# Performance work log

Hardware: AMD Instinct MI355X
Metric: run time of the kernel (lower is better)

## Reference

```python
import jax, jax.numpy as jnp
import numpy as np

N = 100000   # n_nodes (= ninput, identity features)
E = 1600000  # edges per adjacency (avg degree 16)
H = 128      # nhid
EPS = 1e-12


def setup_inputs() -> dict:
    key = jax.random.key(0)
    ks = jax.random.split(key, 24)
    inp = {
        'adj1_rows': jax.random.randint(ks[0], (E,), 0, N),
        'adj1_cols': jax.random.randint(ks[1], (E,), 0, N),
        'adj1_vals': jax.random.uniform(ks[2], (E,), jnp.float32) / 16.0,
        'adj2_rows': jax.random.randint(ks[3], (E,), 0, N),
        'adj2_cols': jax.random.randint(ks[4], (E,), 0, N),
        'adj2_vals': jax.random.uniform(ks[5], (E,), jnp.float32) / 16.0,
    }
    s = 1.0 / np.sqrt(H)
    inp['w1'] = jax.random.uniform(ks[6], (N, H), jnp.float32, -s, s)
    for i in range(2, 10):
        inp[f'w{i}'] = jax.random.uniform(ks[5 + i], (H, H), jnp.float32, -s, s)
    s2 = 1.0 / np.sqrt(2 * H)
    inp['m1'] = jax.random.uniform(ks[15], (H, 2 * H), jnp.float32, -s, s)
    inp['b1'] = jnp.zeros((2 * H,), jnp.float32)
    inp['m2'] = jax.random.uniform(ks[16], (2 * H, 2 * H), jnp.float32, -s2, s2)
    inp['b2'] = jnp.zeros((2 * H,), jnp.float32)
    inp['m3'] = jax.random.uniform(ks[17], (2 * H, 1), jnp.float32, -s2, s2)
    inp['b3'] = jnp.zeros((1,), jnp.float32)
    return inp


def _spmm(rows, cols, vals, x):
    # sparse [N,N] @ dense [N,H] via gather + segment_sum
    return jax.ops.segment_sum(vals[:, None] * x[cols], rows, num_segments=N)


def _l2norm(x):
    # F.normalize(x, p=2, dim=1)
    n = jnp.sqrt(jnp.sum(x * x, axis=1, keepdims=True))
    return x / jnp.maximum(n, EPS)


def _mlp(x, m1, b1, m2, b2, m3, b3):
    # dropout inactive (eval mode) for deterministic reference
    h = jax.nn.relu(x @ m1 + b1)
    h = jax.nn.relu(h @ m2 + b2)
    return h @ m3 + b3  # [N,1]


def _branch(rows, cols, vals, w1, ws, mlp_params):
    x = jax.nn.relu(_spmm(rows, cols, vals, w1))
    x = _l2norm(x)
    score = _mlp(x, *mlp_params)
    for i, w in enumerate(ws):
        x = jax.nn.relu(_spmm(rows, cols, vals, x @ w))
        if i < len(ws) - 1:  # last layer (gc9) is relu only, no normalize
            x = _l2norm(x)
        score = score + _mlp(x, *mlp_params)
    return score


def reference(adj1_rows, adj1_cols, adj1_vals, adj2_rows, adj2_cols, adj2_vals,
              w1, w2, w3, w4, w5, w6, w7, w8, w9,
              m1, b1, m2, b2, m3, b3):
    ws = [w2, w3, w4, w5, w6, w7, w8, w9]
    mlp_params = (m1, b1, m2, b2, m3, b3)
    score1 = _branch(adj1_rows, adj1_cols, adj1_vals, w1, ws, mlp_params)
    score2 = _branch(adj2_rows, adj2_cols, adj2_vals, w1, ws, mlp_params)
    return score1 * score2  # [N,1]
```

## Files before the change

kernel.cpp:

```cpp
#include <hip/hip_runtime.h>
#include <hip/hip_fp16.h>

#define NN 100000
#define NE 1600000
#define HD 128
#define HD2 256

typedef unsigned int u32;
typedef unsigned short u16;
typedef _Float16 half8 __attribute__((ext_vector_type(8)));
typedef float floatx4 __attribute__((ext_vector_type(4)));

static inline int cdiv(int a, int b){ return (a + b - 1) / b; }

__device__ __forceinline__ u32 split_pack(float v){
  __half h;
  if(fabsf(v) < 6.103515625e-05f) h = __ushort_as_half((u16)0);
  else h = __float2half_rn(v);
  float hf = __half2float(h);
  __half l = __float2half_rn((v - hf) * 4096.0f);
  return (u32)__half_as_ushort(h) | ((u32)__half_as_ushort(l) << 16);
}

__global__ void k_zero_int(int* __restrict__ p, int n){
  int i = blockIdx.x * 256 + threadIdx.x;
  if(i < n) p[i] = 0;
}

__global__ void k_zero_f(float* __restrict__ p, int n){
  int i = blockIdx.x * 256 + threadIdx.x;
  if(i < n) p[i] = 0.f;
}

__global__ void k_hist2(const int* __restrict__ r0, const int* __restrict__ r1,
                        int* __restrict__ cnt){
  int e = blockIdx.x * 256 + threadIdx.x;
  if(e < NE){
    const int* rows = blockIdx.y ? r1 : r0;
    atomicAdd(&cnt[blockIdx.y * NN + rows[e]], 1);
  }
}

__global__ void k_scan1b(const int* __restrict__ cnt, int* __restrict__ p0,
                         int* __restrict__ p1, int* __restrict__ sums, int n){
  __shared__ int sh[256];
  int z = blockIdx.y;
  const int* c = cnt + z * n;
  int* part = z ? p1 : p0;
  int* sm = sums + z * 128;
  int tid = threadIdx.x;
  int base = blockIdx.x * 1024 + tid * 4;
  int v0 = (base + 0 < n) ? c[base + 0] : 0;
  int v1 = (base + 1 < n) ? c[base + 1] : 0;
  int v2 = (base + 2 < n) ? c[base + 2] : 0;
  int v3 = (base + 3 < n) ? c[base + 3] : 0;
  int s = v0 + v1 + v2 + v3;
  sh[tid] = s;
  __syncthreads();
  for(int d = 1; d < 256; d <<= 1){
    int t = (tid >= d) ? sh[tid - d] : 0;
    __syncthreads();
    sh[tid] += t;
    __syncthreads();
  }
  int excl = sh[tid] - s;
  if(tid == 255) sm[blockIdx.x] = sh[255];
  if(base + 0 < n) part[base + 0] = excl;
  if(base + 1 < n) part[base + 1] = excl + v0;
  if(base + 2 < n) part[base + 2] = excl + v0 + v1;
  if(base + 3 < n) part[base + 3] = excl + v0 + v1 + v2;
}

__global__ void k_scan2b(int* __restrict__ sums, int nb){
  __shared__ int sh[128];
  int* s = sums + blockIdx.x * 128;
  int tid = threadIdx.x;
  int v = (tid < nb) ? s[tid] : 0;
  sh[tid] = v;
  __syncthreads();
  for(int d = 1; d < 128; d <<= 1){
    int t = (tid >= d) ? sh[tid - d] : 0;
    __syncthreads();
    sh[tid] += t;
    __syncthreads();
  }
  if(tid < nb) s[tid] = sh[tid] - v;
}

__global__ void k_scan3b(int* __restrict__ r0, int* __restrict__ r1,
                         int* __restrict__ cursor, const int* __restrict__ sums, int n){
  int z = blockIdx.y;
  int* rowptr = z ? r1 : r0;
  int* cur = cursor + z * n;
  int off = sums[z * 128 + blockIdx.x];
  int tid = threadIdx.x;
  int base = blockIdx.x * 1024 + tid * 4;
  #pragma unroll
  for(int j = 0; j < 4; j++){
    int idx = base + j;
    if(idx < n){ int r = rowptr[idx] + off; rowptr[idx] = r; cur[idx] = r; }
  }
  if(blockIdx.x == 0 && tid == 0) rowptr[n] = NE;
}

__global__ void k_scatter2(const int* __restrict__ r0, const int* __restrict__ c0,
                           const float* __restrict__ v0,
                           const int* __restrict__ r1, const int* __restrict__ c1,
                           const float* __restrict__ v1,
                           int* __restrict__ cursor,
                           int* __restrict__ oc0, float* __restrict__ ov0,
                           int* __restrict__ oc1, float* __restrict__ ov1){
  int e = blockIdx.x * 256 + threadIdx.x;
  if(e < NE){
    int z = blockIdx.y;
    const int* rows = z ? r1 : r0;
    const int* cols = z ? c1 : c0;
    const float* vals = z ? v1 : v0;
    int* cur = cursor + z * NN;
    int* ocol = z ? oc1 : oc0;
    float* oval = z ? ov1 : ov0;
    int r = rows[e];
    int pp = atomicAdd(&cur[r], 1);
    ocol[pp] = cols[e];
    oval[pp] = vals[e];
  }
}

__global__ void k_splitw(const float* __restrict__ W, u32* __restrict__ out,
                         int K, int N, int total){
  int idx = blockIdx.x * 256 + threadIdx.x;
  if(idx < total){
    int n = idx / K, k = idx - n * K;
    out[idx] = split_pack(W[(size_t)k * N + n]);
  }
}

template<bool NORM>
__global__ void k_spmm(const int* __restrict__ rp0, const int* __restrict__ col0,
                       const float* __restrict__ val0,
                       const int* __restrict__ rp1, const int* __restrict__ col1,
                       const float* __restrict__ val1,
                       const float* __restrict__ X0, const float* __restrict__ X1,
                       u32* __restrict__ outpk){
  int z = blockIdx.z;
  const int* rowptr = z ? rp1 : rp0;
  const int* col    = z ? col1 : col0;
  const float* val  = z ? val1 : val0;
  const float* X    = z ? X1 : X0;
  int node = (blockIdx.x << 2) + (threadIdx.x >> 6);
  int lane = threadIdx.x & 63;
  if(node >= NN) return;
  int s = rowptr[node], e = rowptr[node + 1];
  float ax = 0.f, ay = 0.f, bx = 0.f, by = 0.f;
  float cx = 0.f, cy = 0.f, dx = 0.f, dy = 0.f;
  int i = s;
  for(; i + 15 < e; i += 16){
    int c[16]; float v[16]; float2 xx[16];
    #pragma unroll
    for(int j = 0; j < 16; j++){ c[j] = col[i + j]; v[j] = val[i + j]; }
    #pragma unroll
    for(int j = 0; j < 16; j++) xx[j] = *(const float2*)(X + (size_t)c[j] * HD + lane * 2);
    #pragma unroll
    for(int j = 0; j < 16; j += 4){
      ax += v[j] * xx[j].x + v[j+1] * xx[j+1].x;
      ay += v[j] * xx[j].y + v[j+1] * xx[j+1].y;
      bx += v[j+2] * xx[j+2].x + v[j+3] * xx[j+3].x;
      by += v[j+2] * xx[j+2].y + v[j+3] * xx[j+3].y;
    }
  }
  for(; i + 3 < e; i += 4){
    int   e0 = col[i],   e1 = col[i + 1], e2 = col[i + 2], e3 = col[i + 3];
    float f0 = val[i],   f1 = val[i + 1], f2 = val[i + 2], f3 = val[i + 3];
    float2 x0 = *(const float2*)(X + (size_t)e0 * HD + lane * 2);
    float2 x1 = *(const float2*)(X + (size_t)e1 * HD + lane * 2);
    float2 x2 = *(const float2*)(X + (size_t)e2 * HD + lane * 2);
    float2 x3 = *(const float2*)(X + (size_t)e3 * HD + lane * 2);
    ax += f0 * x0.x + f1 * x1.x;  ay += f0 * x0.y + f1 * x1.y;
    bx += f2 * x2.x + f3 * x3.x;  by += f2 * x2.y + f3 * x3.y;
  }
  for(; i < e; i++){
    int c = col[i]; float v = val[i];
    float2 xv = *(const float2*)(X + (size_t)c * HD + lane * 2);
    ax += v * xv.x; ay += v * xv.y;
  }
  ax += bx + cx + dx;
  ay += by + cy + dy;
  ax = fmaxf(ax, 0.f);
  ay = fmaxf(ay, 0.f);
  if(NORM){
    float ss = ax * ax + ay * ay;
    #pragma unroll
    for(int o = 32; o >= 1; o >>= 1) ss += __shfl_xor(ss, o, 64);
    float scale = 1.f / fmaxf(sqrtf(ss), 1e-12f);
    ax *= scale; ay *= scale;
  }
  size_t gnode = (size_t)(z * NN + node);
  *(uint2*)(outpk + gnode * HD + lane * 2) = make_uint2(split_pack(ax), split_pack(ay));
}

template<int MODE>
__launch_bounds__(256, 2)
__global__ void k_mfma_gemm(const u32* __restrict__ Apk, const u32* __restrict__ Btpk,
                            const float* __restrict__ bias, float* __restrict__ Yout,
                            u32* __restrict__ Hout, const float* __restrict__ m3,
                            float* __restrict__ score, int M, int K, int N){
  __shared__ unsigned short As_h[128 * 40], As_l[128 * 40];
  __shared__ unsigned short Bs_h[128 * 40], Bs_l[128 * 40];
  const int tid = threadIdx.x;
  const int lane = tid & 63, wid = tid >> 6;
  const int lm = lane & 15, lg = lane >> 4;
  const int mq = (wid & 1) * 64, nq = (wid >> 1) * 64;
  const int m0 = blockIdx.x * 128, n0 = blockIdx.y * 128;

  floatx4 accA[4][4], accB[4][4];
  #pragma unroll
  for(int i = 0; i < 4; i++)
    #pragma unroll
    for(int j = 0; j < 4; j++){
      accA[i][j] = (floatx4){0.f, 0.f, 0.f, 0.f};
      accB[i][j] = (floatx4){0.f, 0.f, 0.f, 0.f};
    }

  for(int k0 = 0; k0 < K; k0 += 32){
    uint4 av[4], bv[4];
    #pragma unroll
    for(int j = 0; j < 4; j++){
      int li = tid + j * 256;
      int row = li >> 3, kc = (li & 7) * 4;
      int ar = m0 + row; if(ar >= M) ar = M - 1;
      av[j] = *(const uint4*)(Apk + (size_t)ar * K + k0 + kc);
      bv[j] = *(const uint4*)(Btpk + (size_t)(n0 + row) * K + k0 + kc);
    }
    __syncthreads();
    #pragma unroll
    for(int j = 0; j < 4; j++){
      int li = tid + j * 256;
      int row = li >> 3, kc = (li & 7) * 4;
      int base = row * 40 + kc;
      ushort4 h, l;
      h.x = (u16)(av[j].x & 0xffff); l.x = (u16)(av[j].x >> 16);
      h.y = (u16)(av[j].y & 0xffff); l.y = (u16)(av[j].y >> 16);
      h.z = (u16)(av[j].z & 0xffff); l.z = (u16)(av[j].z >> 16);
      h.w = (u16)(av[j].w & 0xffff); l.w = (u16)(av[j].w >> 16);
      *(ushort4*)&As_h[base] = h;
      *(ushort4*)&As_l[base] = l;
      h.x = (u16)(bv[j].x & 0xffff); l.x = (u16)(bv[j].x >> 16);
      h.y = (u16)(bv[j].y & 0xffff); l.y = (u16)(bv[j].y >> 16);
      h.z = (u16)(bv[j].z & 0xffff); l.z = (u16)(bv[j].z >> 16);
      h.w = (u16)(bv[j].w & 0xffff); l.w = (u16)(bv[j].w >> 16);
      *(ushort4*)&Bs_h[base] = h;
      *(ushort4*)&Bs_l[base] = l;
    }
    __syncthreads();

    half8 fa_h[4], fa_l[4], fb_h[4], fb_l[4];
    #pragma unroll
    for(int s = 0; s < 4; s++){
      int ra = (mq + s * 16 + lm) * 40 + lg * 8;
      fa_h[s] = *(const half8*)&As_h[ra];
      fa_l[s] = *(const half8*)&As_l[ra];
      int rb = (nq + s * 16 + lm) * 40 + lg * 8;
      fb_h[s] = *(const half8*)&Bs_h[rb];
      fb_l[s] = *(const half8*)&Bs_l[rb];
    }
    #pragma unroll
    for(int i = 0; i < 4; i++)
      #pragma unroll
      for(int j = 0; j < 4; j++){
        accA[i][j] = __builtin_amdgcn_mfma_f32_16x16x32_f16(fa_h[i], fb_h[j], accA[i][j], 0, 0, 0);
        accB[i][j] = __builtin_amdgcn_mfma_f32_16x16x32_f16(fa_h[i], fb_l[j], accB[i][j], 0, 0, 0);
        accB[i][j] = __builtin_amdgcn_mfma_f32_16x16x32_f16(fa_l[i], fb_h[j], accB[i][j], 0, 0, 0);
      }
  }

  const float inv4096 = 1.f / 4096.f;
  if(MODE == 0){
    #pragma unroll
    for(int i = 0; i < 4; i++)
      #pragma unroll
      for(int r = 0; r < 4; r++){
        int m = m0 + mq + i * 16 + lg * 4 + r;
        if(m < M){
          #pragma unroll
          for(int j = 0; j < 4; j++){
            int c = n0 + nq + j * 16 + lm;
            Yout[(size_t)m * N + c] = accA[i][j][r] + accB[i][j][r] * inv4096;
          }
        }
      }
  } else if(MODE == 1){
    #pragma unroll
    for(int i = 0; i < 4; i++)
      #pragma unroll
      for(int r = 0; r < 4; r++){
        int m = m0 + mq + i * 16 + lg * 4 + r;
        if(m < M){
          #pragma unroll
          for(int j = 0; j < 4; j++){
            int c = n0 + nq + j * 16 + lm;
            float v = fmaxf(accA[i][j][r] + accB[i][j][r] * inv4096 + bias[c], 0.f);
            Hout[(size_t)m * N + c] = split_pack(v);
          }
        }
      }
  } else {
    #pragma unroll
    for(int i = 0; i < 4; i++)
      #pragma unroll
      for(int r = 0; r < 4; r++){
        float s = 0.f;
        #pragma unroll
        for(int j = 0; j < 4; j++){
          int c = n0 + nq + j * 16 + lm;
          float v = fmaxf(accA[i][j][r] + accB[i][j][r] * inv4096 + bias[c], 0.f);
          s = fmaf(v, m3[c], s);
        }
        s += __shfl_xor(s, 1, 64);
        s += __shfl_xor(s, 2, 64);
        s += __shfl_xor(s, 4, 64);
        s += __shfl_xor(s, 8, 64);
        int m = m0 + mq + i * 16 + lg * 4 + r;
        if(lm == 0 && m < M) atomicAdd(&score[m], s);
      }
  }
}

__global__ void k_final(const float* __restrict__ sc, const float* __restrict__ b3,
                        float* __restrict__ out){
  int i = blockIdx.x * 256 + threadIdx.x;
  if(i < NN){
    float b = 9.f * b3[0];
    out[i] = (sc[i] + b) * (sc[NN + i] + b);
  }
}

extern "C" void kernel_launch(void* const* d_in, const int* in_sizes, int n_in,
                              void* d_out, int out_size, void* d_ws, size_t ws_size,
                              hipStream_t stream){
  const int*   a1r = (const int*)d_in[0];
  const int*   a1c = (const int*)d_in[1];
  const float* a1v = (const float*)d_in[2];
  const int*   a2r = (const int*)d_in[3];
  const int*   a2c = (const int*)d_in[4];
  const float* a2v = (const float*)d_in[5];
  const float* w1  = (const float*)d_in[6];
  const float* w[8];
  for(int i = 0; i < 8; i++) w[i] = (const float*)d_in[7 + i];
  const float* m1 = (const float*)d_in[15];
  const float* b1 = (const float*)d_in[16];
  const float* m2 = (const float*)d_in[17];
  const float* b2 = (const float*)d_in[18];
  const float* m3 = (const float*)d_in[19];
  const float* b3 = (const float*)d_in[20];
  float* out = (float*)d_out;

  char* base = (char*)d_ws;
  size_t off = 0;
  auto alloc = [&](size_t bytes) -> char* {
    char* r = base + off;
    off += (bytes + 255) & ~(size_t)255;
    return r;
  };
  int*   c1ptr = (int*)  alloc((size_t)(NN + 1) * 4);
  int*   c1col = (int*)  alloc((size_t)NE * 4);
  float* c1val = (float*)alloc((size_t)NE * 4);
  int*   c2ptr = (int*)  alloc((size_t)(NN + 1) * 4);
  int*   c2col = (int*)  alloc((size_t)NE * 4);
  float* c2val = (float*)alloc((size_t)NE * 4);
  int*   cursor= (int*)  alloc((size_t)2 * NN * 4);
  int*   sums  = (int*)  alloc(1024);
  float* sc    = (float*)alloc((size_t)2 * NN * 4);
  u32*   wtpk[8];
  for(int i = 0; i < 8; i++) wtpk[i] = (u32*)alloc((size_t)HD * HD * 4);
  u32*   m1tpk = (u32*)alloc((size_t)HD2 * HD * 4);
  u32*   m2tpk = (u32*)alloc((size_t)HD2 * HD2 * 4);

  size_t fixed = off;
  size_t need_batched = fixed + (((size_t)2*NN*HD*4 + 255) & ~(size_t)255)
                              + (((size_t)2*NN*HD2*4 + 255) & ~(size_t)255);
  bool batched = (ws_size >= need_batched);
  int MB = batched ? 2 * NN : NN;
  u32*   xpk  = (u32*)alloc((size_t)MB * HD * 4);
  u32*   h1pk = (u32*)alloc((size_t)MB * HD2 * 4);
  float* y = (float*)h1pk;

  hipLaunchKernelGGL(k_zero_int, dim3(cdiv(2 * NN, 256)), dim3(256), 0, stream, cursor, 2 * NN);
  hipLaunchKernelGGL(k_hist2, dim3(cdiv(NE, 256), 2), dim3(256), 0, stream, a1r, a2r, cursor);
  const int SCAN_BLOCKS = cdiv(NN, 1024);
  hipLaunchKernelGGL(k_scan1b, dim3(SCAN_BLOCKS, 2), dim3(256), 0, stream, cursor, c1ptr, c2ptr, sums, NN);
  hipLaunchKernelGGL(k_scan2b, dim3(2), dim3(128), 0, stream, sums, SCAN_BLOCKS);
  hipLaunchKernelGGL(k_scan3b, dim3(SCAN_BLOCKS, 2), dim3(256), 0, stream, c1ptr, c2ptr, cursor, sums, NN);
  hipLaunchKernelGGL(k_scatter2, dim3(cdiv(NE, 256), 2), dim3(256), 0, stream,
                     a1r, a1c, a1v, a2r, a2c, a2v, cursor, c1col, c1val, c2col, c2val);

  auto splitw = [&](const float* W, u32* o, int K, int N){
    int total = K * N;
    hipLaunchKernelGGL(k_splitw, dim3(cdiv(total, 256)), dim3(256), 0, stream, W, o, K, N, total);
  };
  for(int i = 0; i < 8; i++) splitw(w[i], wtpk[i], HD, HD);
  splitw(m1, m1tpk, HD, HD2);
  splitw(m2, m2tpk, HD2, HD2);

  hipLaunchKernelGGL(k_zero_f, dim3(cdiv(2 * NN, 256)), dim3(256), 0, stream, sc, 2 * NN);

  auto mlp = [&](int M, float* score){
    int gx = cdiv(M, 128);
    hipLaunchKernelGGL((k_mfma_gemm<1>), dim3(gx, 2), dim3(256), 0, stream,
                       xpk, m1tpk, b1, (float*)nullptr, h1pk,
                       (const float*)nullptr, (float*)nullptr, M, HD, HD2);
    hipLaunchKernelGGL((k_mfma_gemm<2>), dim3(gx, 2), dim3(256), 0, stream,
                       h1pk, m2tpk, b2, (float*)nullptr, (u32*)nullptr,
                       m3, score, M, HD2, HD2);
  };

  if(batched){
    hipLaunchKernelGGL((k_spmm<true>), dim3(cdiv(NN, 4), 1, 2), dim3(256), 0, stream,
                       c1ptr, c1col, c1val, c2ptr, c2col, c2val, w1, w1, xpk);
    mlp(2 * NN, sc);
    for(int i = 0; i < 8; i++){
      hipLaunchKernelGGL((k_mfma_gemm<0>), dim3(cdiv(2 * NN, 128), 1), dim3(256), 0, stream,
                         xpk, wtpk[i], (const float*)nullptr, y, (u32*)nullptr,
                         (const float*)nullptr, (float*)nullptr, 2 * NN, HD, HD);
      if(i < 7)
        hipLaunchKernelGGL((k_spmm<true>), dim3(cdiv(NN, 4), 1, 2), dim3(256), 0, stream,
                           c1ptr, c1col, c1val, c2ptr, c2col, c2val,
                           y, y + (size_t)NN * HD, xpk);
      else
        hipLaunchKernelGGL((k_spmm<false>), dim3(cdiv(NN, 4), 1, 2), dim3(256), 0, stream,
                           c1ptr, c1col, c1val, c2ptr, c2col, c2val,
                           y, y + (size_t)NN * HD, xpk);
      mlp(2 * NN, sc);
    }
  } else {
    for(int b = 0; b < 2; b++){
      const int* rp = b ? c2ptr : c1ptr;
      const int* cc = b ? c2col : c1col;
      const float* vv = b ? c2val : c1val;
      float* score = sc + (size_t)b * NN;
      hipLaunchKernelGGL((k_spmm<true>), dim3(cdiv(NN, 4), 1, 1), dim3(256), 0, stream,
                         rp, cc, vv, rp, cc, vv, w1, w1, xpk);
      mlp(NN, score);
      for(int i = 0; i < 8; i++){
        hipLaunchKernelGGL((k_mfma_gemm<0>), dim3(cdiv(NN, 128), 1), dim3(256), 0, stream,
                           xpk, wtpk[i], (const float*)nullptr, y, (u32*)nullptr,
                           (const float*)nullptr, (float*)nullptr, NN, HD, HD);
        if(i < 7)
          hipLaunchKernelGGL((k_spmm<true>), dim3(cdiv(NN, 4), 1, 1), dim3(256), 0, stream,
                             rp, cc, vv, rp, cc, vv, y, y, xpk);
        else
          hipLaunchKernelGGL((k_spmm<false>), dim3(cdiv(NN, 4), 1, 1), dim3(256), 0, stream,
                             rp, cc, vv, rp, cc, vv, y, y, xpk);
        mlp(NN, score);
      }
    }
  }

  hipLaunchKernelGGL(k_final, dim3(cdiv(NN, 256)), dim3(256), 0, stream, sc, b3, out);
}
```

Before: 4.847 ms.

## Split packed hi/lo fp16 planes and stage GEMM tiles via direct global-to-LDS loads

Result: no change. 4.917 ms (+1.4%).

```diff
diff --git a/kernel.cpp b/kernel.cpp
--- a/kernel.cpp
+++ b/kernel.cpp
@@ -20,6 +20,12 @@
   float hf = __half2float(h);
   __half l = __float2half_rn((v - hf) * 4096.0f);
   return (u32)__half_as_ushort(h) | ((u32)__half_as_ushort(l) << 16);
+}
+
+__device__ __forceinline__ void glds16(const u16* g, u16* s){
+  auto* gp = (const __attribute__((address_space(1))) u32*)(g);
+  auto* sp = (__attribute__((address_space(3))) u32*)(s);
+  __builtin_amdgcn_global_load_lds(gp, sp, 16, 0, 0);
 }
 
 __global__ void k_zero_int(int* __restrict__ p, int n){
@@ -126,12 +132,14 @@
   }
 }
 
-__global__ void k_splitw(const float* __restrict__ W, u32* __restrict__ out,
-                         int K, int N, int total){
+__global__ void k_splitw(const float* __restrict__ W, u16* __restrict__ oh,
+                         u16* __restrict__ ol, int K, int N, int total){
   int idx = blockIdx.x * 256 + threadIdx.x;
   if(idx < total){
     int n = idx / K, k = idx - n * K;
-    out[idx] = split_pack(W[(size_t)k * N + n]);
+    u32 p = split_pack(W[(size_t)k * N + n]);
+    oh[idx] = (u16)(p & 0xffffu);
+    ol[idx] = (u16)(p >> 16);
   }
 }
 
@@ -141,7 +149,7 @@
                        const int* __restrict__ rp1, const int* __restrict__ col1,
                        const float* __restrict__ val1,
                        const float* __restrict__ X0, const float* __restrict__ X1,
-                       u32* __restrict__ outpk){
+                       u16* __restrict__ outh, u16* __restrict__ outl){
   int z = blockIdx.z;
   const int* rowptr = z ? rp1 : rp0;
   const int* col    = z ? col1 : col0;
@@ -152,7 +160,6 @@
   if(node >= NN) return;
   int s = rowptr[node], e = rowptr[node + 1];
   float ax = 0.f, ay = 0.f, bx = 0.f, by = 0.f;
-  float cx = 0.f, cy = 0.f, dx = 0.f, dy = 0.f;
   int i = s;
   for(; i + 15 < e; i += 16){
     int c[16]; float v[16]; float2 xx[16];
@@ -183,8 +190,7 @@
     float2 xv = *(const float2*)(X + (size_t)c * HD + lane * 2);
     ax += v * xv.x; ay += v * xv.y;
   }
-  ax += bx + cx + dx;
-  ay += by + cy + dy;
+  ax += bx; ay += by;
   ax = fmaxf(ax, 0.f);
   ay = fmaxf(ay, 0.f);
   if(NORM){
@@ -194,23 +200,33 @@
     float scale = 1.f / fmaxf(sqrtf(ss), 1e-12f);
     ax *= scale; ay *= scale;
   }
-  size_t gnode = (size_t)(z * NN + node);
-  *(uint2*)(outpk + gnode * HD + lane * 2) = make_uint2(split_pack(ax), split_pack(ay));
+  u32 p0 = split_pack(ax), p1 = split_pack(ay);
+  u32 hw = (p0 & 0xffffu) | (p1 << 16);
+  u32 lw = (p0 >> 16) | (p1 & 0xffff0000u);
+  size_t o = (size_t)(z * NN + node) * HD + lane * 2;
+  *(u32*)(outh + o) = hw;
+  *(u32*)(outl + o) = lw;
 }
 
 template<int MODE>
 __launch_bounds__(256, 2)
-__global__ void k_mfma_gemm(const u32* __restrict__ Apk, const u32* __restrict__ Btpk,
+__global__ void k_mfma_gemm(const u16* __restrict__ Ah, const u16* __restrict__ Al,
+                            const u16* __restrict__ Bh, const u16* __restrict__ Bl,
                             const float* __restrict__ bias, float* __restrict__ Yout,
-                            u32* __restrict__ Hout, const float* __restrict__ m3,
-                            float* __restrict__ score, int M, int K, int N){
-  __shared__ unsigned short As_h[128 * 40], As_l[128 * 40];
-  __shared__ unsigned short Bs_h[128 * 40], Bs_l[128 * 40];
+                            u16* __restrict__ Hh, u16* __restrict__ Hl,
+                            const float* __restrict__ m3, float* __restrict__ score,
+                            int M, int K, int N){
+  __shared__ __attribute__((aligned(16))) u16 sAh[128 * 32];
+  __shared__ __attribute__((aligned(16))) u16 sAl[128 * 32];
+  __shared__ __attribute__((aligned(16))) u16 sBh[128 * 32];
+  __shared__ __attribute__((aligned(16))) u16 sBl[128 * 32];
   const int tid = threadIdx.x;
   const int lane = tid & 63, wid = tid >> 6;
   const int lm = lane & 15, lg = lane >> 4;
   const int mq = (wid & 1) * 64, nq = (wid >> 1) * 64;
   const int m0 = blockIdx.x * 128, n0 = blockIdx.y * 128;
+  const int l4 = lane >> 2, lc3 = lane & 3;
+  const int ca8 = ((lg ^ ((lm >> 2) & 3))) * 8;
 
   floatx4 accA[4][4], accB[4][4];
   #pragma unroll
@@ -222,46 +238,31 @@
     }
 
   for(int k0 = 0; k0 < K; k0 += 32){
-    uint4 av[4], bv[4];
-    #pragma unroll
-    for(int j = 0; j < 4; j++){
-      int li = tid + j * 256;
-      int row = li >> 3, kc = (li & 7) * 4;
-      int ar = m0 + row; if(ar >= M) ar = M - 1;
-      av[j] = *(const uint4*)(Apk + (size_t)ar * K + k0 + kc);
-      bv[j] = *(const uint4*)(Btpk + (size_t)(n0 + row) * K + k0 + kc);
+    if(k0) __syncthreads();
+    #pragma unroll
+    for(int t = 0; t < 2; t++){
+      int row = wid * 32 + t * 16 + l4;
+      int cph = (lc3 ^ ((row >> 2) & 3)) * 8;
+      int arow = m0 + row; if(arow >= M) arow = M - 1;
+      size_t ga = (size_t)arow * K + k0 + cph;
+      size_t gb = (size_t)(n0 + row) * K + k0 + cph;
+      int ld = (wid * 2 + t) * 512;
+      glds16(Ah + ga, sAh + ld);
+      glds16(Al + ga, sAl + ld);
+      glds16(Bh + gb, sBh + ld);
+      glds16(Bl + gb, sBl + ld);
     }
     __syncthreads();
-    #pragma unroll
-    for(int j = 0; j < 4; j++){
-      int li = tid + j * 256;
-      int row = li >> 3, kc = (li & 7) * 4;
-      int base = row * 40 + kc;
-      ushort4 h, l;
-      h.x = (u16)(av[j].x & 0xffff); l.x = (u16)(av[j].x >> 16);
-      h.y = (u16)(av[j].y & 0xffff); l.y = (u16)(av[j].y >> 16);
-      h.z = (u16)(av[j].z & 0xffff); l.z = (u16)(av[j].z >> 16);
-      h.w = (u16)(av[j].w & 0xffff); l.w = (u16)(av[j].w >> 16);
-      *(ushort4*)&As_h[base] = h;
-      *(ushort4*)&As_l[base] = l;
-      h.x = (u16)(bv[j].x & 0xffff); l.x = (u16)(bv[j].x >> 16);
-      h.y = (u16)(bv[j].y & 0xffff); l.y = (u16)(bv[j].y >> 16);
-      h.z = (u16)(bv[j].z & 0xffff); l.z = (u16)(bv[j].z >> 16);
-      h.w = (u16)(bv[j].w & 0xffff); l.w = (u16)(bv[j].w >> 16);
-      *(ushort4*)&Bs_h[base] = h;
-      *(ushort4*)&Bs_l[base] = l;
-    }
-    __syncthreads();
 
     half8 fa_h[4], fa_l[4], fb_h[4], fb_l[4];
     #pragma unroll
     for(int s = 0; s < 4; s++){
-      int ra = (mq + s * 16 + lm) * 40 + lg * 8;
-      fa_h[s] = *(const half8*)&As_h[ra];
-      fa_l[s] = *(const half8*)&As_l[ra];
-      int rb = (nq + s * 16 + lm) * 40 + lg * 8;
-      fb_h[s] = *(const half8*)&Bs_h[rb];
-      fb_l[s] = *(const half8*)&Bs_l[rb];
+      int ra = (mq + s * 16 + lm) * 32 + ca8;
+      fa_h[s] = *(const half8*)&sAh[ra];
+      fa_l[s] = *(const half8*)&sAl[ra];
+      int rb = (nq + s * 16 + lm) * 32 + ca8;
+      fb_h[s] = *(const half8*)&sBh[rb];
+      fb_l[s] = *(const half8*)&sBl[rb];
     }
     #pragma unroll
     for(int i = 0; i < 4; i++)
@@ -299,7 +300,9 @@
           for(int j = 0; j < 4; j++){
             int c = n0 + nq + j * 16 + lm;
             float v = fmaxf(accA[i][j][r] + accB[i][j][r] * inv4096 + bias[c], 0.f);
-            Hout[(size_t)m * N + c] = split_pack(v);
+            u32 p = split_pack(v);
+            Hh[(size_t)m * N + c] = (u16)(p & 0xffffu);
+            Hl[(size_t)m * N + c] = (u16)(p >> 16);
           }
         }
       }
@@ -370,19 +373,27 @@
   int*   cursor= (int*)  alloc((size_t)2 * NN * 4);
   int*   sums  = (int*)  alloc(1024);
   float* sc    = (float*)alloc((size_t)2 * NN * 4);
-  u32*   wtpk[8];
-  for(int i = 0; i < 8; i++) wtpk[i] = (u32*)alloc((size_t)HD * HD * 4);
-  u32*   m1tpk = (u32*)alloc((size_t)HD2 * HD * 4);
-  u32*   m2tpk = (u32*)alloc((size_t)HD2 * HD2 * 4);
+  u16 *wth[8], *wtl[8];
+  for(int i = 0; i < 8; i++){
+    wth[i] = (u16*)alloc((size_t)HD * HD * 2);
+    wtl[i] = (u16*)alloc((size_t)HD * HD * 2);
+  }
+  u16* m1th = (u16*)alloc((size_t)HD2 * HD * 2);
+  u16* m1tl = (u16*)alloc((size_t)HD2 * HD * 2);
+  u16* m2th = (u16*)alloc((size_t)HD2 * HD2 * 2);
+  u16* m2tl = (u16*)alloc((size_t)HD2 * HD2 * 2);
 
   size_t fixed = off;
-  size_t need_batched = fixed + (((size_t)2*NN*HD*4 + 255) & ~(size_t)255)
-                              + (((size_t)2*NN*HD2*4 + 255) & ~(size_t)255);
+  size_t need_batched = fixed
+      + 2 * ((((size_t)2 * NN * HD * 2) + 255) & ~(size_t)255)
+      + 2 * ((((size_t)2 * NN * HD2 * 2) + 255) & ~(size_t)255);
   bool batched = (ws_size >= need_batched);
   int MB = batched ? 2 * NN : NN;
-  u32*   xpk  = (u32*)alloc((size_t)MB * HD * 4);
-  u32*   h1pk = (u32*)alloc((size_t)MB * HD2 * 4);
-  float* y = (float*)h1pk;
+  u16*   xh  = (u16*)alloc((size_t)MB * HD * 2);
+  u16*   xl  = (u16*)alloc((size_t)MB * HD * 2);
+  u16*   h1h = (u16*)alloc((size_t)MB * HD2 * 2);
+  u16*   h1l = (u16*)alloc((size_t)MB * HD2 * 2);
+  float* y = (float*)h1h;
 
   hipLaunchKernelGGL(k_zero_int, dim3(cdiv(2 * NN, 256)), dim3(256), 0, stream, cursor, 2 * NN);
   hipLaunchKernelGGL(k_hist2, dim3(cdiv(NE, 256), 2), dim3(256), 0, stream, a1r, a2r, cursor);
@@ -393,42 +404,43 @@
   hipLaunchKernelGGL(k_scatter2, dim3(cdiv(NE, 256), 2), dim3(256), 0, stream,
                      a1r, a1c, a1v, a2r, a2c, a2v, cursor, c1col, c1val, c2col, c2val);
 
-  auto splitw = [&](const float* W, u32* o, int K, int N){
+  auto splitw = [&](const float* W, u16* oh, u16* ol, int K, int N){
     int total = K * N;
-    hipLaunchKernelGGL(k_splitw, dim3(cdiv(total, 256)), dim3(256), 0, stream, W, o, K, N, total);
+    hipLaunchKernelGGL(k_splitw, dim3(cdiv(total, 256)), dim3(256), 0, stream, W, oh, ol, K, N, total);
   };
-  for(int i = 0; i < 8; i++) splitw(w[i], wtpk[i], HD, HD);
-  splitw(m1, m1tpk, HD, HD2);
-  splitw(m2, m2tpk, HD2, HD2);
+  for(int i = 0; i < 8; i++) splitw(w[i], wth[i], wtl[i], HD, HD);
+  splitw(m1, m1th, m1tl, HD, HD2);
+  splitw(m2, m2th, m2tl, HD2, HD2);
 
   hipLaunchKernelGGL(k_zero_f, dim3(cdiv(2 * NN, 256)), dim3(256), 0, stream, sc, 2 * NN);
 
   auto mlp = [&](int M, float* score){
     int gx = cdiv(M, 128);
     hipLaunchKernelGGL((k_mfma_gemm<1>), dim3(gx, 2), dim3(256), 0, stream,
-                       xpk, m1tpk, b1, (float*)nullptr, h1pk,
+                       xh, xl, m1th, m1tl, b1, (float*)nullptr, h1h, h1l,
                        (const float*)nullptr, (float*)nullptr, M, HD, HD2);
     hipLaunchKernelGGL((k_mfma_gemm<2>), dim3(gx, 2), dim3(256), 0, stream,
-                       h1pk, m2tpk, b2, (float*)nullptr, (u32*)nullptr,
+                       h1h, h1l, m2th, m2tl, b2, (float*)nullptr, (u16*)nullptr, (u16*)nullptr,
                        m3, score, M, HD2, HD2);
   };
 
   if(batched){
     hipLaunchKernelGGL((k_spmm<true>), dim3(cdiv(NN, 4), 1, 2), dim3(256), 0, stream,
-                       c1ptr, c1col, c1val, c2ptr, c2col, c2val, w1, w1, xpk);
+                       c1ptr, c1col, c1val, c2ptr, c2col, c2val, w1, w1, xh, xl);
     mlp(2 * NN, sc);
     for(int i = 0; i < 8; i++){
       hipLaunchKernelGGL((k_mfma_gemm<0>), dim3(cdiv(2 * NN, 128), 1), dim3(256), 0, stream,
-                         xpk, wtpk[i], (const float*)nullptr, y, (u32*)nullptr,
+                         xh, xl, wth[i], wtl[i], (const float*)nullptr, y,
+                         (u16*)nullptr, (u16*)nullptr,
                          (const float*)nullptr, (float*)nullptr, 2 * NN, HD, HD);
       if(i < 7)
         hipLaunchKernelGGL((k_spmm<true>), dim3(cdiv(NN, 4), 1, 2), dim3(256), 0, stream,
                            c1ptr, c1col, c1val, c2ptr, c2col, c2val,
-                           y, y + (size_t)NN * HD, xpk);
+                           y, y + (size_t)NN * HD, xh, xl);
       else
         hipLaunchKernelGGL((k_spmm<false>), dim3(cdiv(NN, 4), 1, 2), dim3(256), 0, stream,
                            c1ptr, c1col, c1val, c2ptr, c2col, c2val,
-                           y, y + (size_t)NN * HD, xpk);
+                           y, y + (size_t)NN * HD, xh, xl);
       mlp(2 * NN, sc);
     }
   } else {
@@ -438,18 +450,19 @@
       const float* vv = b ? c2val : c1val;
       float* score = sc + (size_t)b * NN;
       hipLaunchKernelGGL((k_spmm<true>), dim3(cdiv(NN, 4), 1, 1), dim3(256), 0, stream,
-                         rp, cc, vv, rp, cc, vv, w1, w1, xpk);
+                         rp, cc, vv, rp, cc, vv, w1, w1, xh, xl);
       mlp(NN, score);
       for(int i = 0; i < 8; i++){
         hipLaunchKernelGGL((k_mfma_gemm<0>), dim3(cdiv(NN, 128), 1), dim3(256), 0, stream,
-                           xpk, wtpk[i], (const float*)nullptr, y, (u32*)nullptr,
+                           xh, xl, wth[i], wtl[i], (const float*)nullptr, y,
+                           (u16*)nullptr, (u16*)nullptr,
                            (const float*)nullptr, (float*)nullptr, NN, HD, HD);
         if(i < 7)
           hipLaunchKernelGGL((k_spmm<true>), dim3(cdiv(NN, 4), 1, 1), dim3(256), 0, stream,
-                             rp, cc, vv, rp, cc, vv, y, y, xpk);
+                             rp, cc, vv, rp, cc, vv, y, y, xh, xl);
         else
           hipLaunchKernelGGL((k_spmm<false>), dim3(cdiv(NN, 4), 1, 1), dim3(256), 0, stream,
-                             rp, cc, vv, rp, cc, vv, y, y, xpk);
+                             rp, cc, vv, rp, cc, vv, y, y, xh, xl);
         mlp(NN, score);
       }
     }
```

## Interleave edge col/val, fuse layer GEMM with MLP first layer, drop batching

Applied to the files above, without the earlier changes.

Result: faster. 4.713 ms (-2.8%).

```diff
diff --git a/kernel.cpp b/kernel.cpp
--- a/kernel.cpp
+++ b/kernel.cpp
@@ -108,8 +108,7 @@
                            const int* __restrict__ r1, const int* __restrict__ c1,
                            const float* __restrict__ v1,
                            int* __restrict__ cursor,
-                           int* __restrict__ oc0, float* __restrict__ ov0,
-                           int* __restrict__ oc1, float* __restrict__ ov1){
+                           uint2* __restrict__ e0, uint2* __restrict__ e1){
   int e = blockIdx.x * 256 + threadIdx.x;
   if(e < NE){
     int z = blockIdx.y;
@@ -117,12 +116,10 @@
     const int* cols = z ? c1 : c0;
     const float* vals = z ? v1 : v0;
     int* cur = cursor + z * NN;
-    int* ocol = z ? oc1 : oc0;
-    float* oval = z ? ov1 : ov0;
+    uint2* ecv = z ? e1 : e0;
     int r = rows[e];
     int pp = atomicAdd(&cur[r], 1);
-    ocol[pp] = cols[e];
-    oval[pp] = vals[e];
+    ecv[pp] = make_uint2((u32)cols[e], __float_as_uint(vals[e]));
   }
 }
 
@@ -136,55 +133,46 @@
 }
 
 template<bool NORM>
-__global__ void k_spmm(const int* __restrict__ rp0, const int* __restrict__ col0,
-                       const float* __restrict__ val0,
-                       const int* __restrict__ rp1, const int* __restrict__ col1,
-                       const float* __restrict__ val1,
-                       const float* __restrict__ X0, const float* __restrict__ X1,
-                       u32* __restrict__ outpk){
-  int z = blockIdx.z;
-  const int* rowptr = z ? rp1 : rp0;
-  const int* col    = z ? col1 : col0;
-  const float* val  = z ? val1 : val0;
-  const float* X    = z ? X1 : X0;
+__global__ void k_spmm(const int* __restrict__ rowptr, const uint2* __restrict__ ecv,
+                       const float* __restrict__ X, u32* __restrict__ outpk){
   int node = (blockIdx.x << 2) + (threadIdx.x >> 6);
   int lane = threadIdx.x & 63;
   if(node >= NN) return;
   int s = rowptr[node], e = rowptr[node + 1];
   float ax = 0.f, ay = 0.f, bx = 0.f, by = 0.f;
-  float cx = 0.f, cy = 0.f, dx = 0.f, dy = 0.f;
   int i = s;
   for(; i + 15 < e; i += 16){
-    int c[16]; float v[16]; float2 xx[16];
-    #pragma unroll
-    for(int j = 0; j < 16; j++){ c[j] = col[i + j]; v[j] = val[i + j]; }
-    #pragma unroll
-    for(int j = 0; j < 16; j++) xx[j] = *(const float2*)(X + (size_t)c[j] * HD + lane * 2);
+    uint2 ee[16]; float2 xx[16];
+    #pragma unroll
+    for(int j = 0; j < 16; j++) ee[j] = ecv[i + j];
+    #pragma unroll
+    for(int j = 0; j < 16; j++) xx[j] = *(const float2*)(X + (size_t)ee[j].x * HD + lane * 2);
     #pragma unroll
     for(int j = 0; j < 16; j += 4){
-      ax += v[j] * xx[j].x + v[j+1] * xx[j+1].x;
-      ay += v[j] * xx[j].y + v[j+1] * xx[j+1].y;
-      bx += v[j+2] * xx[j+2].x + v[j+3] * xx[j+3].x;
-      by += v[j+2] * xx[j+2].y + v[j+3] * xx[j+3].y;
+      ax += __uint_as_float(ee[j].y)   * xx[j].x   + __uint_as_float(ee[j+1].y) * xx[j+1].x;
+      ay += __uint_as_float(ee[j].y)   * xx[j].y   + __uint_as_float(ee[j+1].y) * xx[j+1].y;
+      bx += __uint_as_float(ee[j+2].y) * xx[j+2].x + __uint_as_float(ee[j+3].y) * xx[j+3].x;
+      by += __uint_as_float(ee[j+2].y) * xx[j+2].y + __uint_as_float(ee[j+3].y) * xx[j+3].y;
     }
   }
   for(; i + 3 < e; i += 4){
-    int   e0 = col[i],   e1 = col[i + 1], e2 = col[i + 2], e3 = col[i + 3];
-    float f0 = val[i],   f1 = val[i + 1], f2 = val[i + 2], f3 = val[i + 3];
-    float2 x0 = *(const float2*)(X + (size_t)e0 * HD + lane * 2);
-    float2 x1 = *(const float2*)(X + (size_t)e1 * HD + lane * 2);
-    float2 x2 = *(const float2*)(X + (size_t)e2 * HD + lane * 2);
-    float2 x3 = *(const float2*)(X + (size_t)e3 * HD + lane * 2);
-    ax += f0 * x0.x + f1 * x1.x;  ay += f0 * x0.y + f1 * x1.y;
-    bx += f2 * x2.x + f3 * x3.x;  by += f2 * x2.y + f3 * x3.y;
+    uint2 f0 = ecv[i], f1 = ecv[i+1], f2 = ecv[i+2], f3 = ecv[i+3];
+    float2 x0 = *(const float2*)(X + (size_t)f0.x * HD + lane * 2);
+    float2 x1 = *(const float2*)(X + (size_t)f1.x * HD + lane * 2);
+    float2 x2 = *(const float2*)(X + (size_t)f2.x * HD + lane * 2);
+    float2 x3 = *(const float2*)(X + (size_t)f3.x * HD + lane * 2);
+    ax += __uint_as_float(f0.y) * x0.x + __uint_as_float(f1.y) * x1.x;
+    ay += __uint_as_float(f0.y) * x0.y + __uint_as_float(f1.y) * x1.y;
+    bx += __uint_as_float(f2.y) * x2.x + __uint_as_float(f3.y) * x3.x;
+    by += __uint_as_float(f2.y) * x2.y + __uint_as_float(f3.y) * x3.y;
   }
   for(; i < e; i++){
-    int c = col[i]; float v = val[i];
-    float2 xv = *(const float2*)(X + (size_t)c * HD + lane * 2);
-    ax += v * xv.x; ay += v * xv.y;
-  }
-  ax += bx + cx + dx;
-  ay += by + cy + dy;
+    uint2 f0 = ecv[i];
+    float2 xv = *(const float2*)(X + (size_t)f0.x * HD + lane * 2);
+    ax += __uint_as_float(f0.y) * xv.x;
+    ay += __uint_as_float(f0.y) * xv.y;
+  }
+  ax += bx; ay += by;
   ax = fmaxf(ax, 0.f);
   ay = fmaxf(ay, 0.f);
   if(NORM){
@@ -194,23 +182,31 @@
     float scale = 1.f / fmaxf(sqrtf(ss), 1e-12f);
     ax *= scale; ay *= scale;
   }
-  size_t gnode = (size_t)(z * NN + node);
-  *(uint2*)(outpk + gnode * HD + lane * 2) = make_uint2(split_pack(ax), split_pack(ay));
+  *(uint2*)(outpk + (size_t)node * HD + lane * 2) = make_uint2(split_pack(ax), split_pack(ay));
 }
 
 template<int MODE>
 __launch_bounds__(256, 2)
 __global__ void k_mfma_gemm(const u32* __restrict__ Apk, const u32* __restrict__ Btpk,
+                            const u32* __restrict__ Bt1pk,
                             const float* __restrict__ bias, float* __restrict__ Yout,
                             u32* __restrict__ Hout, const float* __restrict__ m3,
                             float* __restrict__ score, int M, int K, int N){
-  __shared__ unsigned short As_h[128 * 40], As_l[128 * 40];
-  __shared__ unsigned short Bs_h[128 * 40], Bs_l[128 * 40];
+  __shared__ u16 As_h[128 * 40], As_l[128 * 40];
+  __shared__ u16 Bs_h[128 * 40], Bs_l[128 * 40];
   const int tid = threadIdx.x;
   const int lane = tid & 63, wid = tid >> 6;
   const int lm = lane & 15, lg = lane >> 4;
   const int mq = (wid & 1) * 64, nq = (wid >> 1) * 64;
-  const int m0 = blockIdx.x * 128, n0 = blockIdx.y * 128;
+  const int m0 = blockIdx.x * 128;
+  int n0 = blockIdx.y * 128;
+  const u32* Bt = Btpk;
+  bool m0path = true;
+  if(MODE == 3){
+    m0path = (blockIdx.y == 0);
+    if(m0path){ n0 = 0; }
+    else      { n0 = (blockIdx.y - 1) * 128; Bt = Bt1pk; }
+  }
 
   floatx4 accA[4][4], accB[4][4];
   #pragma unroll
@@ -229,9 +225,9 @@
       int row = li >> 3, kc = (li & 7) * 4;
       int ar = m0 + row; if(ar >= M) ar = M - 1;
       av[j] = *(const uint4*)(Apk + (size_t)ar * K + k0 + kc);
-      bv[j] = *(const uint4*)(Btpk + (size_t)(n0 + row) * K + k0 + kc);
-    }
-    __syncthreads();
+      bv[j] = *(const uint4*)(Bt + (size_t)(n0 + row) * K + k0 + kc);
+    }
+    if(k0) __syncthreads();
     #pragma unroll
     for(int j = 0; j < 4; j++){
       int li = tid + j * 256;
@@ -274,7 +270,8 @@
   }
 
   const float inv4096 = 1.f / 4096.f;
-  if(MODE == 0){
+  if(MODE == 0 || (MODE == 3 && m0path)){
+    int ldy = (MODE == 3) ? HD : N;
     #pragma unroll
     for(int i = 0; i < 4; i++)
       #pragma unroll
@@ -284,11 +281,12 @@
           #pragma unroll
           for(int j = 0; j < 4; j++){
             int c = n0 + nq + j * 16 + lm;
-            Yout[(size_t)m * N + c] = accA[i][j][r] + accB[i][j][r] * inv4096;
+            Yout[(size_t)m * ldy + c] = accA[i][j][r] + accB[i][j][r] * inv4096;
           }
         }
       }
-  } else if(MODE == 1){
+  } else if(MODE == 1 || MODE == 3){
+    int ldh = (MODE == 3) ? HD2 : N;
     #pragma unroll
     for(int i = 0; i < 4; i++)
       #pragma unroll
@@ -299,7 +297,7 @@
           for(int j = 0; j < 4; j++){
             int c = n0 + nq + j * 16 + lm;
             float v = fmaxf(accA[i][j][r] + accB[i][j][r] * inv4096 + bias[c], 0.f);
-            Hout[(size_t)m * N + c] = split_pack(v);
+            Hout[(size_t)m * ldh + c] = split_pack(v);
           }
         }
       }
@@ -362,11 +360,9 @@
     return r;
   };
   int*   c1ptr = (int*)  alloc((size_t)(NN + 1) * 4);
-  int*   c1col = (int*)  alloc((size_t)NE * 4);
-  float* c1val = (float*)alloc((size_t)NE * 4);
   int*   c2ptr = (int*)  alloc((size_t)(NN + 1) * 4);
-  int*   c2col = (int*)  alloc((size_t)NE * 4);
-  float* c2val = (float*)alloc((size_t)NE * 4);
+  uint2* ecv1  = (uint2*)alloc((size_t)NE * 8);
+  uint2* ecv2  = (uint2*)alloc((size_t)NE * 8);
   int*   cursor= (int*)  alloc((size_t)2 * NN * 4);
   int*   sums  = (int*)  alloc(1024);
   float* sc    = (float*)alloc((size_t)2 * NN * 4);
@@ -374,15 +370,11 @@
   for(int i = 0; i < 8; i++) wtpk[i] = (u32*)alloc((size_t)HD * HD * 4);
   u32*   m1tpk = (u32*)alloc((size_t)HD2 * HD * 4);
   u32*   m2tpk = (u32*)alloc((size_t)HD2 * HD2 * 4);
-
-  size_t fixed = off;
-  size_t need_batched = fixed + (((size_t)2*NN*HD*4 + 255) & ~(size_t)255)
-                              + (((size_t)2*NN*HD2*4 + 255) & ~(size_t)255);
-  bool batched = (ws_size >= need_batched);
-  int MB = batched ? 2 * NN : NN;
-  u32*   xpk  = (u32*)alloc((size_t)MB * HD * 4);
-  u32*   h1pk = (u32*)alloc((size_t)MB * HD2 * 4);
-  float* y = (float*)h1pk;
+  u32*   xpk   = (u32*)alloc((size_t)NN * HD * 4);
+  u32*   h1pk  = (u32*)alloc((size_t)NN * HD2 * 4);
+  size_t need_ded = off + (((size_t)NN * HD * 4 + 255) & ~(size_t)255);
+  bool ded_y = (ws_size >= need_ded);
+  float* y = ded_y ? (float*)alloc((size_t)NN * HD * 4) : (float*)h1pk;
 
   hipLaunchKernelGGL(k_zero_int, dim3(cdiv(2 * NN, 256)), dim3(256), 0, stream, cursor, 2 * NN);
   hipLaunchKernelGGL(k_hist2, dim3(cdiv(NE, 256), 2), dim3(256), 0, stream, a1r, a2r, cursor);
@@ -391,7 +383,7 @@
   hipLaunchKernelGGL(k_scan2b, dim3(2), dim3(128), 0, stream, sums, SCAN_BLOCKS);
   hipLaunchKernelGGL(k_scan3b, dim3(SCAN_BLOCKS, 2), dim3(256), 0, stream, c1ptr, c2ptr, cursor, sums, NN);
   hipLaunchKernelGGL(k_scatter2, dim3(cdiv(NE, 256), 2), dim3(256), 0, stream,
-                     a1r, a1c, a1v, a2r, a2c, a2v, cursor, c1col, c1val, c2col, c2val);
+                     a1r, a1c, a1v, a2r, a2c, a2v, cursor, ecv1, ecv2);
 
   auto splitw = [&](const float* W, u32* o, int K, int N){
     int total = K * N;
@@ -400,57 +392,62 @@
   for(int i = 0; i < 8; i++) splitw(w[i], wtpk[i], HD, HD);
   splitw(m1, m1tpk, HD, HD2);
   splitw(m2, m2tpk, HD2, HD2);
-
   hipLaunchKernelGGL(k_zero_f, dim3(cdiv(2 * NN, 256)), dim3(256), 0, stream, sc, 2 * NN);
 
-  auto mlp = [&](int M, float* score){
-    int gx = cdiv(M, 128);
-    hipLaunchKernelGGL((k_mfma_gemm<1>), dim3(gx, 2), dim3(256), 0, stream,
-                       xpk, m1tpk, b1, (float*)nullptr, h1pk,
-                       (const float*)nullptr, (float*)nullptr, M, HD, HD2);
-    hipLaunchKernelGGL((k_mfma_gemm<2>), dim3(gx, 2), dim3(256), 0, stream,
-                       h1pk, m2tpk, b2, (float*)nullptr, (u32*)nullptr,
-                       m3, score, M, HD2, HD2);
-  };
-
-  if(batched){
-    hipLaunchKernelGGL((k_spmm<true>), dim3(cdiv(NN, 4), 1, 2), dim3(256), 0, stream,
-                       c1ptr, c1col, c1val, c2ptr, c2col, c2val, w1, w1, xpk);
-    mlp(2 * NN, sc);
-    for(int i = 0; i < 8; i++){
-      hipLaunchKernelGGL((k_mfma_gemm<0>), dim3(cdiv(2 * NN, 128), 1), dim3(256), 0, stream,
-                         xpk, wtpk[i], (const float*)nullptr, y, (u32*)nullptr,
-                         (const float*)nullptr, (float*)nullptr, 2 * NN, HD, HD);
-      if(i < 7)
-        hipLaunchKernelGGL((k_spmm<true>), dim3(cdiv(NN, 4), 1, 2), dim3(256), 0, stream,
-                           c1ptr, c1col, c1val, c2ptr, c2col, c2val,
-                           y, y + (size_t)NN * HD, xpk);
-      else
-        hipLaunchKernelGGL((k_spmm<false>), dim3(cdiv(NN, 4), 1, 2), dim3(256), 0, stream,
-                           c1ptr, c1col, c1val, c2ptr, c2col, c2val,
-                           y, y + (size_t)NN * HD, xpk);
-      mlp(2 * NN, sc);
-    }
-  } else {
-    for(int b = 0; b < 2; b++){
-      const int* rp = b ? c2ptr : c1ptr;
-      const int* cc = b ? c2col : c1col;
-      const float* vv = b ? c2val : c1val;
-      float* score = sc + (size_t)b * NN;
-      hipLaunchKernelGGL((k_spmm<true>), dim3(cdiv(NN, 4), 1, 1), dim3(256), 0, stream,
-                         rp, cc, vv, rp, cc, vv, w1, w1, xpk);
-      mlp(NN, score);
+  const int GX = cdiv(NN, 128);
+  auto mode1 = [&](){
+    hipLaunchKernelGGL((k_mfma_gemm<1>), dim3(GX, 2), dim3(256), 0, stream,
+                       xpk, m1tpk, (const u32*)nullptr, b1, (float*)nullptr, h1pk,
+                       (const float*)nullptr, (float*)nullptr, NN, HD, HD2);
+  };
+  auto mode2 = [&](float* score){
+    hipLaunchKernelGGL((k_mfma_gemm<2>), dim3(GX, 2), dim3(256), 0, stream,
+                       h1pk, m2tpk, (const u32*)nullptr, b2, (float*)nullptr, (u32*)nullptr,
+                       m3, score, NN, HD2, HD2);
+  };
+  auto gemm0 = [&](int i){
+    hipLaunchKernelGGL((k_mfma_gemm<0>), dim3(GX, 1), dim3(256), 0, stream,
+                       xpk, wtpk[i], (const u32*)nullptr, (const float*)nullptr, y, (u32*)nullptr,
+                       (const float*)nullptr, (float*)nullptr, NN, HD, HD);
+  };
+  auto fused01 = [&](int i){
+    hipLaunchKernelGGL((k_mfma_gemm<3>), dim3(GX, 3), dim3(256), 0, stream,
+                       xpk, wtpk[i], m1tpk, b1, y, h1pk,
+                       (const float*)nullptr, (float*)nullptr, NN, HD, 0);
+  };
+
+  for(int b = 0; b < 2; b++){
+    const int* rp = b ? c2ptr : c1ptr;
+    const uint2* ecv = b ? ecv2 : ecv1;
+    float* score = sc + (size_t)b * NN;
+    hipLaunchKernelGGL((k_spmm<true>), dim3(cdiv(NN, 4)), dim3(256), 0, stream,
+                       rp, ecv, w1, xpk);
+    if(ded_y){
       for(int i = 0; i < 8; i++){
-        hipLaunchKernelGGL((k_mfma_gemm<0>), dim3(cdiv(NN, 128), 1), dim3(256), 0, stream,
-                           xpk, wtpk[i], (const float*)nullptr, y, (u32*)nullptr,
-                           (const float*)nullptr, (float*)nullptr, NN, HD, HD);
+        fused01(i);
+        mode2(score);
         if(i < 7)
-          hipLaunchKernelGGL((k_spmm<true>), dim3(cdiv(NN, 4), 1, 1), dim3(256), 0, stream,
-                             rp, cc, vv, rp, cc, vv, y, y, xpk);
+          hipLaunchKernelGGL((k_spmm<true>),  dim3(cdiv(NN, 4)), dim3(256), 0, stream,
+                             rp, ecv, y, xpk);
         else
-          hipLaunchKernelGGL((k_spmm<false>), dim3(cdiv(NN, 4), 1, 1), dim3(256), 0, stream,
-                             rp, cc, vv, rp, cc, vv, y, y, xpk);
-        mlp(NN, score);
+          hipLaunchKernelGGL((k_spmm<false>), dim3(cdiv(NN, 4)), dim3(256), 0, stream,
+                             rp, ecv, y, xpk);
+      }
+      mode1();
+      mode2(score);
+    } else {
+      mode1();
+      mode2(score);
+      for(int i = 0; i < 8; i++){
+        gemm0(i);
+        if(i < 7)
+          hipLaunchKernelGGL((k_spmm<true>),  dim3(cdiv(NN, 4)), dim3(256), 0, stream,
+                             rp, ecv, y, xpk);
+        else
+          hipLaunchKernelGGL((k_spmm<false>), dim3(cdiv(NN, 4)), dim3(256), 0, stream,
+                             rp, ecv, y, xpk);
+        mode1();
+        mode2(score);
       }
     }
   }
```
